# Kernel tuning notes

Measured on AMD Instinct MI355X. Metric: run time of the kernel, lower is better.

The kernel has to match this reference:

```python
import jax, jax.numpy as jnp
import numpy as np

B, T, J, D = 64, 2048, 128, 256

def setup_inputs() -> dict:
    key = jax.random.key(0)
    k1, k2, k3 = jax.random.split(key, 3)
    H = jax.random.normal(k1, (B, T, D), dtype=jnp.float32)
    U = jax.random.normal(k2, (B, J, D), dtype=jnp.float32)
    w = jax.random.normal(k3, (3 * D, 1), dtype=jnp.float32) * 0.05
    return {"H": H, "U": U, "w": w}


def reference(H, U, w):
    # Original: tile H to (B,T,J,D), tile U to (B,T,J,D), concat [H,U,H*U] -> (B,T,J,3D),
    # then dot with w (3D,1) and squeeze -> (B,T,J).
    # Equivalent trilinear form without materializing the tiled tensor:
    # S[b,t,j] = H[b,t]@w1 + U[b,j]@w2 + (H[b,t]*w3)@U[b,j]
    d = H.shape[-1]
    wv = w[:, 0]
    w1, w2, w3 = wv[:d], wv[d:2 * d], wv[2 * d:]
    s_h = jnp.einsum('btd,d->bt', H, w1)          # (B,T)
    s_u = jnp.einsum('bjd,d->bj', U, w2)          # (B,J)
    s_hu = jnp.einsum('btd,bjd->btj', H * w3, U)  # (B,T,J)
    return s_h[:, :, None] + s_u[:, None, :] + s_hu
```

## Files before the change

### kernel.cpp

```cpp
#include <hip/hip_runtime.h>
#include <stdint.h>

#define Bb 64
#define Tt 2048
#define Jj 128
#define Dd 256


typedef __attribute__((ext_vector_type(8))) __bf16 bf16x8;
typedef __attribute__((ext_vector_type(8))) unsigned short ushort8v;
typedef __attribute__((ext_vector_type(4))) float f32x4;

__device__ __forceinline__ unsigned short f2bf(float f) {
    unsigned int u = __builtin_bit_cast(unsigned int, f);
    u += 0x7FFFu + ((u >> 16) & 1u);
    return (unsigned short)(u >> 16);
}

__device__ __forceinline__ bf16x8 pack8(const float4& a0, const float4& a1) {
    bf16x8 r;
    r[0] = (__bf16)a0.x; r[1] = (__bf16)a0.y; r[2] = (__bf16)a0.z; r[3] = (__bf16)a0.w;
    r[4] = (__bf16)a1.x; r[5] = (__bf16)a1.y; r[6] = (__bf16)a1.z; r[7] = (__bf16)a1.w;
    return r;
}

__global__ __launch_bounds__(512, 4)
void sim_fused(const float* __restrict__ H, const float* __restrict__ U,
               const float* __restrict__ w, float* __restrict__ out) {
    __shared__ ushort8v lUp[4608];
    __shared__ float    lsuP[8 * Jj];
    __shared__ float    lsu[Jj];

    const int tid   = threadIdx.x;
    const int wid   = tid >> 6;
    const int lane  = tid & 63;
    const int row16 = lane & 15;
    const int quad  = lane >> 4;

    const int o     = blockIdx.x;
    const int b     = (o & 7) * 8 + ((o >> 3) & 7);
    const int mbase = (o >> 6) * 256;

    const float* Hbase = H + ((size_t)(b * Tt + mbase + wid * 16 + row16)) * Dd + quad * 8;
    float4 hb0[6], hb1[6];
#pragma unroll
    for (int p = 0; p < 6; ++p) {
        const float* np = Hbase + (size_t)((p >> 3) * 128 * Dd) + (p & 7) * 32;
        hb0[p] = *(const float4*)(np);
        hb1[p] = *(const float4*)(np + 4);
    }

    const int k0 = wid * 32 + quad * 8;
    const float4 w1a = *(const float4*)(w + k0);
    const float4 w1b = *(const float4*)(w + k0 + 4);
    const float4 w2a = *(const float4*)(w + Dd + k0);
    const float4 w2b = *(const float4*)(w + Dd + k0 + 4);
    const float4 w3a = *(const float4*)(w + 2 * Dd + k0);
    const float4 w3b = *(const float4*)(w + 2 * Dd + k0 + 4);

    const float* Ubase = U + (size_t)b * Jj * Dd;
    float sup[8];
#pragma unroll
    for (int p = 0; p < 8; ++p) {
        const float* up = Ubase + (size_t)(p * 16 + row16) * Dd + k0;
        const float4 u0 = *(const float4*)(up);
        const float4 u1 = *(const float4*)(up + 4);
        ushort8v s;
        s[0] = f2bf(u0.x * w3a.x); s[1] = f2bf(u0.y * w3a.y);
        s[2] = f2bf(u0.z * w3a.z); s[3] = f2bf(u0.w * w3a.w);
        s[4] = f2bf(u1.x * w3b.x); s[5] = f2bf(u1.y * w3b.y);
        s[6] = f2bf(u1.z * w3b.z); s[7] = f2bf(u1.w * w3b.w);
        lUp[(p * 8 + wid) * 64 + lane] = s;
        sup[p] = u0.x * w2a.x + u0.y * w2a.y + u0.z * w2a.z + u0.w * w2a.w
               + u1.x * w2b.x + u1.y * w2b.y + u1.z * w2b.z + u1.w * w2b.w;
    }
    {
        const bool n0 = row16 == 0;
        ushort8v s;
        s[0] = n0 ? f2bf(w1a.x) : (unsigned short)0;
        s[1] = n0 ? f2bf(w1a.y) : (unsigned short)0;
        s[2] = n0 ? f2bf(w1a.z) : (unsigned short)0;
        s[3] = n0 ? f2bf(w1a.w) : (unsigned short)0;
        s[4] = n0 ? f2bf(w1b.x) : (unsigned short)0;
        s[5] = n0 ? f2bf(w1b.y) : (unsigned short)0;
        s[6] = n0 ? f2bf(w1b.z) : (unsigned short)0;
        s[7] = n0 ? f2bf(w1b.w) : (unsigned short)0;
        lUp[(8 * 8 + wid) * 64 + lane] = s;
    }
#pragma unroll
    for (int p = 0; p < 8; ++p) {
        sup[p] += __shfl_xor(sup[p], 16);
        sup[p] += __shfl_xor(sup[p], 32);
    }
    if (quad == 0) {
#pragma unroll
        for (int p = 0; p < 8; ++p)
            lsuP[wid * Jj + p * 16 + row16] = sup[p];
    }

    f32x4 acc[9];
#pragma unroll
    for (int j = 0; j < 9; ++j) acc[j] = (f32x4){0.f, 0.f, 0.f, 0.f};

    __syncthreads();

    if (tid < Jj) {
        float s = 0.f;
#pragma unroll
        for (int ww = 0; ww < 8; ++ww) s += lsuP[ww * Jj + tid];
        lsu[tid] = s;
    }
    __syncthreads();

#pragma unroll
    for (int mt = 0; mt < 2; ++mt) {
#pragma unroll
        for (int ks = 0; ks < 8; ++ks) {
            const int kk   = mt * 8 + ks;
            const int slot = kk % 6;
            const float4 h0 = hb0[slot];
            const float4 h1 = hb1[slot];
            if (kk < 10) {
                const float* np = Hbase + (size_t)(((kk + 6) >> 3) * 128 * Dd)
                                        + ((kk + 6) & 7) * 32;
                hb0[slot] = *(const float4*)(np);
                hb1[slot] = *(const float4*)(np + 4);
            }

            const bf16x8 af = pack8(h0, h1);
#pragma unroll
            for (int j = 0; j < 9; ++j) {
                const bf16x8 bf = __builtin_bit_cast(bf16x8, lUp[(j * 8 + ks) * 64 + lane]);
                acc[j] = __builtin_amdgcn_mfma_f32_16x16x32_bf16(af, bf, acc[j], 0, 0, 0);
            }
        }

        float shv[4];
#pragma unroll
        for (int rg = 0; rg < 4; ++rg)
            shv[rg] = __shfl(acc[8][rg], quad * 16);

        float* outW = out + ((size_t)(b * Tt + mbase + mt * 128 + wid * 16)) * Jj;
#pragma unroll
        for (int j = 0; j < 8; ++j) {
            const int col = j * 16 + row16;
            const float suv = lsu[col];
#pragma unroll
            for (int rg = 0; rg < 4; ++rg)
                outW[(size_t)(quad * 4 + rg) * Jj + col] = acc[j][rg] + shv[rg] + suv;
        }

        if (mt == 0) {
#pragma unroll
            for (int j = 0; j < 9; ++j) acc[j] = (f32x4){0.f, 0.f, 0.f, 0.f};
        }
    }
}

extern "C" void kernel_launch(void* const* d_in, const int* in_sizes, int n_in,
                              void* d_out, int out_size, void* d_ws, size_t ws_size,
                              hipStream_t stream) {
    const float* H = (const float*)d_in[0];
    const float* U = (const float*)d_in[1];
    const float* w = (const float*)d_in[2];
    float* out = (float*)d_out;
    (void)d_ws; (void)ws_size;

    sim_fused<<<Bb * 8, 512, 0, stream>>>(H, U, w, out);
}
```

Before: 223.4 us.

## Reorganize U staging per row and deepen H prefetch buffer

Each wave now loads whole U rows (its own 16 columns of J) instead of a D-slice of all rows. This lets the w2 dot product be reduced within the wave by shuffles and written directly to shared memory, removing the partial-sum array and one block barrier. The LDS layout for the staged U*w3 fragments is permuted to match. The H register prefetch buffer grows from 6 to 8 slots, so a whole second tile's row is prefetched per k-step. This costs more registers, which could hurt occupancy at 512 threads with a minimum of 4 blocks, and w2/w3 are reloaded per iteration.

```diff
diff --git a/kernel.cpp b/kernel.cpp
--- a/kernel.cpp
+++ b/kernel.cpp
@@ -28,7 +28,6 @@
 void sim_fused(const float* __restrict__ H, const float* __restrict__ U,
                const float* __restrict__ w, float* __restrict__ out) {
     __shared__ ushort8v lUp[4608];
-    __shared__ float    lsuP[8 * Jj];
     __shared__ float    lsu[Jj];
 
     const int tid   = threadIdx.x;
@@ -42,39 +41,38 @@
     const int mbase = (o >> 6) * 256;
 
     const float* Hbase = H + ((size_t)(b * Tt + mbase + wid * 16 + row16)) * Dd + quad * 8;
-    float4 hb0[6], hb1[6];
+    float4 hb0[8], hb1[8];
 #pragma unroll
-    for (int p = 0; p < 6; ++p) {
-        const float* np = Hbase + (size_t)((p >> 3) * 128 * Dd) + (p & 7) * 32;
-        hb0[p] = *(const float4*)(np);
-        hb1[p] = *(const float4*)(np + 4);
+    for (int p = 0; p < 8; ++p) {
+        hb0[p] = *(const float4*)(Hbase + p * 32);
+        hb1[p] = *(const float4*)(Hbase + p * 32 + 4);
     }
 
-    const int k0 = wid * 32 + quad * 8;
-    const float4 w1a = *(const float4*)(w + k0);
-    const float4 w1b = *(const float4*)(w + k0 + 4);
-    const float4 w2a = *(const float4*)(w + Dd + k0);
-    const float4 w2b = *(const float4*)(w + Dd + k0 + 4);
-    const float4 w3a = *(const float4*)(w + 2 * Dd + k0);
-    const float4 w3b = *(const float4*)(w + 2 * Dd + k0 + 4);
-
-    const float* Ubase = U + (size_t)b * Jj * Dd;
-    float sup[8];
+    const float* Urow = U + ((size_t)(b * Jj + wid * 16 + row16)) * Dd + quad * 8;
+    float sup = 0.f;
 #pragma unroll
     for (int p = 0; p < 8; ++p) {
-        const float* up = Ubase + (size_t)(p * 16 + row16) * Dd + k0;
-        const float4 u0 = *(const float4*)(up);
-        const float4 u1 = *(const float4*)(up + 4);
+        const float4 u0 = *(const float4*)(Urow + p * 32);
+        const float4 u1 = *(const float4*)(Urow + p * 32 + 4);
+        const float* w3p = w + 2 * Dd + p * 32 + quad * 8;
+        const float4 w30 = *(const float4*)(w3p);
+        const float4 w31 = *(const float4*)(w3p + 4);
+        const float* w2p = w + Dd + p * 32 + quad * 8;
+        const float4 w20 = *(const float4*)(w2p);
+        const float4 w21 = *(const float4*)(w2p + 4);
         ushort8v s;
-        s[0] = f2bf(u0.x * w3a.x); s[1] = f2bf(u0.y * w3a.y);
-        s[2] = f2bf(u0.z * w3a.z); s[3] = f2bf(u0.w * w3a.w);
-        s[4] = f2bf(u1.x * w3b.x); s[5] = f2bf(u1.y * w3b.y);
-        s[6] = f2bf(u1.z * w3b.z); s[7] = f2bf(u1.w * w3b.w);
-        lUp[(p * 8 + wid) * 64 + lane] = s;
-        sup[p] = u0.x * w2a.x + u0.y * w2a.y + u0.z * w2a.z + u0.w * w2a.w
-               + u1.x * w2b.x + u1.y * w2b.y + u1.z * w2b.z + u1.w * w2b.w;
+        s[0] = f2bf(u0.x * w30.x); s[1] = f2bf(u0.y * w30.y);
+        s[2] = f2bf(u0.z * w30.z); s[3] = f2bf(u0.w * w30.w);
+        s[4] = f2bf(u1.x * w31.x); s[5] = f2bf(u1.y * w31.y);
+        s[6] = f2bf(u1.z * w31.z); s[7] = f2bf(u1.w * w31.w);
+        lUp[(wid * 8 + p) * 64 + lane] = s;
+        sup += u0.x * w20.x + u0.y * w20.y + u0.z * w20.z + u0.w * w20.w
+             + u1.x * w21.x + u1.y * w21.y + u1.z * w21.z + u1.w * w21.w;
     }
     {
+        const int k0 = wid * 32 + quad * 8;
+        const float4 w1a = *(const float4*)(w + k0);
+        const float4 w1b = *(const float4*)(w + k0 + 4);
         const bool n0 = row16 == 0;
         ushort8v s;
         s[0] = n0 ? f2bf(w1a.x) : (unsigned short)0;
@@ -87,16 +85,9 @@
         s[7] = n0 ? f2bf(w1b.w) : (unsigned short)0;
         lUp[(8 * 8 + wid) * 64 + lane] = s;
     }
-#pragma unroll
-    for (int p = 0; p < 8; ++p) {
-        sup[p] += __shfl_xor(sup[p], 16);
-        sup[p] += __shfl_xor(sup[p], 32);
-    }
-    if (quad == 0) {
-#pragma unroll
-        for (int p = 0; p < 8; ++p)
-            lsuP[wid * Jj + p * 16 + row16] = sup[p];
-    }
+    sup += __shfl_xor(sup, 16);
+    sup += __shfl_xor(sup, 32);
+    if (lane < 16) lsu[wid * 16 + lane] = sup;
 
     f32x4 acc[9];
 #pragma unroll
@@ -104,27 +95,16 @@
 
     __syncthreads();
 
-    if (tid < Jj) {
-        float s = 0.f;
-#pragma unroll
-        for (int ww = 0; ww < 8; ++ww) s += lsuP[ww * Jj + tid];
-        lsu[tid] = s;
-    }
-    __syncthreads();
-
 #pragma unroll
     for (int mt = 0; mt < 2; ++mt) {
 #pragma unroll
         for (int ks = 0; ks < 8; ++ks) {
-            const int kk   = mt * 8 + ks;
-            const int slot = kk % 6;
-            const float4 h0 = hb0[slot];
-            const float4 h1 = hb1[slot];
-            if (kk < 10) {
-                const float* np = Hbase + (size_t)(((kk + 6) >> 3) * 128 * Dd)
-                                        + ((kk + 6) & 7) * 32;
-                hb0[slot] = *(const float4*)(np);
-                hb1[slot] = *(const float4*)(np + 4);
+            const float4 h0 = hb0[ks];
+            const float4 h1 = hb1[ks];
+            if (mt == 0) {
+                const float* np = Hbase + (size_t)(128 * Dd) + ks * 32;
+                hb0[ks] = *(const float4*)(np);
+                hb1[ks] = *(const float4*)(np + 4);
             }
 
             const bf16x8 af = pack8(h0, h1);
```

New measurement: 249.0 us. +11.4%, slower.
